# Optimization experiments

Measured on AMD Instinct MI355X. Metric: run time of the kernel, lower is better.

Reference implementation:

```python
import jax, jax.numpy as jnp
import numpy as np

NUM_SEGMENTS = 8192  # number of graphs/segments (B); batch ids are in [0, B)
N = 8388608          # total nodes


def setup_inputs() -> dict:
    key = jax.random.key(0)
    k1, k2 = jax.random.split(key)
    x = jax.random.normal(k1, (N,), dtype=jnp.float32)
    batch = jnp.sort(jax.random.randint(k2, (N,), 0, NUM_SEGMENTS))
    return {"x": x, "batch": batch}


def _sparsemax(x, batch):
    n = x.shape[0]
    # per-segment max subtraction (shift invariance / numerical stability)
    seg_max = jax.ops.segment_max(x, batch, num_segments=NUM_SEGMENTS)
    xs = x - seg_max[batch]

    # segmented descending sort: primary key = batch, secondary = -x
    order = jnp.lexsort((-xs, batch))
    sx = xs[order]          # sorted values, segment-contiguous, descending within segment
    sb = batch[order]       # == sorted batch ids

    # segment sizes and start offsets
    num_nodes = jax.ops.segment_sum(jnp.ones_like(batch), batch, num_segments=NUM_SEGMENTS)
    cum = jnp.concatenate([jnp.zeros((1,), num_nodes.dtype), jnp.cumsum(num_nodes)[:-1]])

    # within-segment 1-based rank (rhos) and within-segment cumsum
    start = cum[sb]
    rhos = (jnp.arange(n) - start + 1).astype(x.dtype)
    c = jnp.cumsum(sx)
    base = jnp.where(start > 0, c[jnp.maximum(start - 1, 0)], jnp.zeros((), x.dtype))
    seg_cumsum = c - base

    # sparsemax support: rho * z_sorted > cumsum - 1
    support = rhos * sx > seg_cumsum - 1.0
    supp_size = jax.ops.segment_sum(support.astype(num_nodes.dtype), sb, num_segments=NUM_SEGMENTS)

    # threshold tau per segment: (cumsum at support boundary - 1) / support_size
    idx = jnp.clip(cum + supp_size - 1, 0, n - 1)
    tau = (seg_cumsum[idx] - 1.0) / jnp.maximum(supp_size, 1).astype(x.dtype)

    return jnp.maximum(xs - tau[batch], 0.0)


def reference(x, batch):
    return _sparsemax(x, batch)
```

## Files before the change

kernel.cpp:

```cpp
#include <hip/hip_runtime.h>


#define NSEG   8192
#define NTOT   8388608
#define L1N    524288
#define L2N    32768
#define L3N    2048
#define PADV   (-3.0e38f)
#define WREG   1216
#define FBB    256

__device__ __forceinline__ int esw(const int e) {
    return (e & ~15) | ((e + (e >> 4)) & 15);
}

__device__ __forceinline__ float sxor(const float v, const int tm) {
    if (tm == 1)
        return __int_as_float(__builtin_amdgcn_mov_dpp(__float_as_int(v), 0xB1, 0xF, 0xF, true));
    if (tm == 2)
        return __int_as_float(__builtin_amdgcn_mov_dpp(__float_as_int(v), 0x4E, 0xF, 0xF, true));
    if (tm == 8)
        return __int_as_float(__builtin_amdgcn_mov_dpp(__float_as_int(v), 0x128, 0xF, 0xF, true));
    return __shfl_xor(v, tm, 64);
}

__device__ __forceinline__ void cs(float& a, float& b, const bool up) {
    const float lo = fminf(a, b), hi = fmaxf(a, b);
    a = up ? hi : lo;
    b = up ? lo : hi;
}
__device__ __forceinline__ void csr(float& a, float& b, const bool up) {
    const bool sw = ((a > b) != up);
    const float t = a;
    a = sw ? b : a;
    b = sw ? t : b;
}

__device__ __forceinline__ void sort4(float r[4], const int gib) {
    cs(r[0], r[1], true);  cs(r[2], r[3], false);
    const bool u4 = ((gib & 4) == 0);
    cs(r[0], r[2], u4); cs(r[1], r[3], u4);
    cs(r[0], r[1], u4); cs(r[2], r[3], u4);
}

template<int K>
__device__ __forceinline__ void bmerge4(float r[4], const int gib) {
    const bool up = ((gib & K) == 0);
    #pragma unroll
    for (int j = K >> 1; j >= 4; j >>= 1) {
        const bool tkm = (up == ((gib & j) == 0));
        const int tm = j >> 2;
        #pragma unroll
        for (int m = 0; m < 4; ++m) {
            const float p = sxor(r[m], tm);
            r[m] = ((r[m] > p) == tkm) ? r[m] : p;
        }
    }
    #pragma unroll
    for (int j = 2; j >= 1; j >>= 1)
        #pragma unroll
        for (int m = 0; m < 4; ++m)
            if ((m & j) == 0) csr(r[m], r[m | j], up);
}

template<int K, int J>
__device__ __forceinline__ void cepm(float r[16]) {
    #pragma unroll
    for (int m = 0; m < 16; ++m)
        if ((m & J) == 0) { const bool up = ((m & K) == 0); cs(r[m], r[m | J], up); }
}
template<int J>
__device__ __forceinline__ void cep(float r[16], const bool up) {
    #pragma unroll
    for (int m = 0; m < 16; ++m)
        if ((m & J) == 0) cs(r[m], r[m | J], up);
}
template<int KD>
__device__ __forceinline__ void kphase16(float r[16], const int l) {
    const bool up = ((l & (KD >> 4)) == 0);
    #pragma unroll
    for (int tm = KD >> 5; tm >= 1; tm >>= 1) {
        const bool tkm = (up == ((l & tm) == 0));
        #pragma unroll
        for (int m = 0; m < 16; ++m) {
            const float p = sxor(r[m], tm);
            r[m] = ((r[m] > p) == tkm) ? r[m] : p;
        }
    }
    if (KD >= 1024) {
        cep<8>(r, up); cep<4>(r, up); cep<2>(r, up); cep<1>(r, up);
    } else {
        #pragma unroll
        for (int j = 8; j >= 1; j >>= 1)
            #pragma unroll
            for (int m = 0; m < 16; ++m)
                if ((m & j) == 0) csr(r[m], r[m | j], up);
    }
}
__device__ __forceinline__ void wsort1024(float r[16], const int l) {
    cepm<2, 1>(r);
    cepm<4, 2>(r); cepm<4, 1>(r);
    cepm<8, 4>(r); cepm<8, 2>(r); cepm<8, 1>(r);
    kphase16<16>(r, l);  kphase16<32>(r, l);  kphase16<64>(r, l);
    kphase16<128>(r, l); kphase16<256>(r, l); kphase16<512>(r, l);
    kphase16<1024>(r, l);
}

__global__ __launch_bounds__(256) void k1_bounds(
    const int* __restrict__ batch, int* __restrict__ starts, const int n)
{
    const int t = blockIdx.x * blockDim.x + threadIdx.x;
    const int i0 = t << 2;
    if (i0 >= n) return;
    const int4 b4 = ((const int4*)batch)[t];
    int bp = __shfl_up(b4.w, 1, 64);
    if (((threadIdx.x & 63) == 0) && i0 > 0) bp = batch[i0 - 1];
    if (i0 == 0) { for (int b = 0; b <= b4.x; ++b) starts[b] = 0; }
    else { for (int b = bp + 1; b <= b4.x; ++b) starts[b] = i0; }
    for (int b = b4.x + 1; b <= b4.y; ++b) starts[b] = i0 + 1;
    for (int b = b4.y + 1; b <= b4.z; ++b) starts[b] = i0 + 2;
    for (int b = b4.z + 1; b <= b4.w; ++b) starts[b] = i0 + 3;
    if (i0 + 4 == n) { for (int b = b4.w + 1; b <= NSEG; ++b) starts[b] = n; }
}

__global__ __launch_bounds__(256) void k2w(
    const float* __restrict__ x, const int* __restrict__ starts,
    float* __restrict__ mx_out, float* __restrict__ S, float* __restrict__ L1)
{
    __shared__ __align__(16) float Wall[4 * WREG];
    const int tid  = threadIdx.x;
    const int lane = tid & 63;
    const int wid  = tid >> 6;
    float* W = Wall + wid * WREG;

    const int b = blockIdx.x * 4 + wid;
    const int s = starts[b], e = starts[b + 1];
    const int n = e - s;
    if (n <= 0) { if (lane == 0) mx_out[b] = 0.0f; return; }

    const bool med = (n > 1024);
    const int  nb  = n - 1024;

    float r[16], rb[4];
    #pragma unroll
    for (int m = 0; m < 16; ++m) { const int i = (m << 6) + lane; r[m] = (i < n) ? x[s + i] : PADV; }
    if (med) {
        #pragma unroll
        for (int m = 0; m < 4; ++m) { const int i = 1024 + (m << 6) + lane; rb[m] = (i < n) ? x[s + i] : PADV; }
    }

    float mx = r[0];
    #pragma unroll
    for (int m = 1; m < 16; ++m) mx = fmaxf(mx, r[m]);
    if (med) {
        #pragma unroll
        for (int m = 0; m < 4; ++m) mx = fmaxf(mx, rb[m]);
    }
    #pragma unroll
    for (int o = 32; o; o >>= 1) mx = fmaxf(mx, sxor(mx, o));
    if (lane == 0) mx_out[b] = mx;

    #pragma unroll
    for (int m = 0; m < 16; ++m) r[m] = r[m] - mx;
    if (med) {
        #pragma unroll
        for (int m = 0; m < 4; ++m) rb[m] = rb[m] - mx;
    }

    wsort1024(r, lane);

    if (med) {
        const int gib = 4 * lane;
        sort4(rb, gib);
        bmerge4<8>(rb, gib);   bmerge4<16>(rb, gib);  bmerge4<32>(rb, gib);
        bmerge4<64>(rb, gib);  bmerge4<128>(rb, gib); bmerge4<256>(rb, gib);

        float tu[16];
        #pragma unroll
        for (int m = 0; m < 16; ++m) {
            const int k  = ((63 - lane) << 4) + (15 - m);
            const int sk = (k >> 2) & 63;
            const float pv = __shfl(rb[(15 - m) & 3], sk, 64);
            const float hi = fmaxf(r[m], pv);
            const float lo = fminf(r[m], pv);
            const bool act = (lane >= 48);
            tu[m] = act ? lo : PADV;
            r[m]  = act ? hi : r[m];
        }
        kphase16<1024>(r, lane);
        #pragma unroll
        for (int tm = 8; tm >= 1; tm >>= 1) {
            const bool tkm = ((lane & tm) == 0);
            #pragma unroll
            for (int m = 0; m < 16; ++m) {
                const float p = sxor(tu[m], tm);
                tu[m] = ((tu[m] > p) == tkm) ? tu[m] : p;
            }
        }
        cep<8>(tu, true); cep<4>(tu, true); cep<2>(tu, true); cep<1>(tu, true);

        #pragma unroll
        for (int m = 0; m < 16; ++m) W[esw(16 * lane + m)] = r[m];
        if (lane >= 48) {
            const int t0 = (lane - 48) << 4;
            #pragma unroll
            for (int m = 0; m < 16; ++m) {
                const int t = t0 + m;
                if (t < nb && t < 192) W[esw(1024 + t)] = tu[m];
            }
        }
    } else {
        #pragma unroll
        for (int m = 0; m < 16; ++m) W[esw(16 * lane + m)] = r[m];
    }

    {
        const int sA = (s + 3) & ~3;
        const int eA = e & ~3;
        if (sA >= eA) {
            for (int i = lane; i < n; i += 64) S[s + i] = W[esw(i)];
        } else {
            if (lane < sA - s) S[s + lane] = W[esw(lane)];
            for (int c = sA + (lane << 2); c < eA; c += 256) {
                const int i = c - s;
                float4 f;
                f.x = W[esw(i)]; f.y = W[esw(i + 1)];
                f.z = W[esw(i + 2)]; f.w = W[esw(i + 3)];
                *(float4*)(S + c) = f;
            }
            if (lane < e - eA) S[eA + lane] = W[esw(eA + lane - s)];
        }
    }

    const int q0 = (s + 15) >> 4, q1 = e >> 4;
    for (int rr = lane; rr < q1 - q0; rr += 64) {
        const int lb = ((q0 + rr) << 4) - s;
        float v[16];
        #pragma unroll
        for (int ii = 0; ii < 16; ++ii) v[ii] = W[esw(lb + ii)];
        float a = 0.0f;
        #pragma unroll
        for (int ii = 0; ii < 16; ++ii) a = a + v[ii];
        L1[q0 + rr] = a;
    }
}

__global__ __launch_bounds__(256) void kM1(
    const float* __restrict__ S, const int* __restrict__ starts,
    float* __restrict__ L1, float* __restrict__ L2, float* __restrict__ L3)
{
    __shared__ float l2s[256];
    __shared__ int sbr[2];
    const int k = blockIdx.x, tid = threadIdx.x;

    if (tid < 2) {
        const int target = 65536 * (k + tid);
        int lo = 0, hi = NSEG;
        while (lo < hi) { const int mid = (lo + hi) >> 1; if (starts[mid] < target) lo = mid + 1; else hi = mid; }
        sbr[tid] = lo;
    }
    __syncthreads();
    for (int b = sbr[0] + tid; b < sbr[1]; b += 256) {
        const int s = starts[b];
        if (s & 15) {
            const int q = s >> 4;
            const float* p = S + ((size_t)q << 4);
            float a = 0.0f;
            #pragma unroll
            for (int i = 0; i < 16; ++i) a = a + p[i];
            L1[q] = a;
        }
    }
    __syncthreads();

    const int q2 = (k << 8) + tid;
    {
        const float* p = L1 + ((size_t)q2 << 4);
        float a = 0.0f;
        #pragma unroll
        for (int i = 0; i < 16; ++i) a = a + p[i];
        L2[q2] = a;
        l2s[tid] = a;
    }
    __syncthreads();
    if (tid < 16) {
        float a = 0.0f;
        #pragma unroll
        for (int i = 0; i < 16; ++i) a = a + l2s[(tid << 4) + i];
        L3[(k << 4) + tid] = a;
    }
}

__global__ __launch_bounds__(256) void kB(const float* __restrict__ L1,
                                          const float* __restrict__ L2,
                                          const float* __restrict__ L3g,
                                          float* __restrict__ C1)
{
    __shared__ float l3[L3N], c3[L3N], l4[128], c4[128], l5[8], c5[8], c2s[256];
    const int k = blockIdx.x, tid = threadIdx.x;

    for (int q = tid; q < L3N; q += 256) l3[q] = L3g[q];
    __syncthreads();
    if (tid < 128) {
        float a = 0.0f;
        for (int i = 0; i < 16; ++i) a = a + l3[tid * 16 + i];
        l4[tid] = a;
    }
    __syncthreads();
    if (tid < 8) {
        float a = 0.0f;
        for (int i = 0; i < 16; ++i) a = a + l4[tid * 16 + i];
        l5[tid] = a;
    }
    __syncthreads();
    if (tid == 0) {
        float a = 0.0f;
        for (int i = 0; i < 8; ++i) { a = a + l5[i]; c5[i] = a; }
    }
    __syncthreads();
    if (tid < 8) {
        const float pre = tid ? c5[tid - 1] : 0.0f;
        float a = 0.0f;
        for (int i = 0; i < 16; ++i) { a = a + l4[tid * 16 + i]; c4[tid * 16 + i] = tid ? (a + pre) : a; }
    }
    __syncthreads();
    if (tid < 128) {
        const float pre = tid ? c4[tid - 1] : 0.0f;
        float a = 0.0f;
        for (int i = 0; i < 16; ++i) { a = a + l3[tid * 16 + i]; c3[tid * 16 + i] = tid ? (a + pre) : a; }
    }
    __syncthreads();
    if (tid < 16) {
        const int q2r = (k << 4) + tid;
        const float pre = q2r ? c3[q2r - 1] : 0.0f;
        const float* p = L2 + ((size_t)q2r << 4);
        float a = 0.0f;
        #pragma unroll
        for (int i = 0; i < 16; ++i) { a = a + p[i]; c2s[(tid << 4) + i] = q2r ? (a + pre) : a; }
    }
    __syncthreads();
    {
        const int p1 = (k << 8) + 1 + tid;
        if (p1 < L2N) {
            const float pre = c2s[tid];
            const float4* pL4 = (const float4*)(L1 + ((size_t)p1 << 4));
            float o[16];
            float a = 0.0f;
            #pragma unroll
            for (int v = 0; v < 4; ++v) {
                const float4 f = pL4[v];
                a = a + f.x; o[4 * v + 0] = a + pre;
                a = a + f.y; o[4 * v + 1] = a + pre;
                a = a + f.z; o[4 * v + 2] = a + pre;
                a = a + f.w; o[4 * v + 3] = a + pre;
            }
            float4* c4p = (float4*)(C1 + ((size_t)p1 << 4));
            #pragma unroll
            for (int v = 0; v < 4; ++v) {
                float4 f;
                f.x = o[4 * v + 0]; f.y = o[4 * v + 1];
                f.z = o[4 * v + 2]; f.w = o[4 * v + 3];
                c4p[v] = f;
            }
        }
        if (k == 0 && tid == 0) {
            float a = 0.0f;
            #pragma unroll
            for (int i = 0; i < 16; ++i) { a = a + L1[i]; C1[i] = a; }
        }
    }
}

__device__ __forceinline__ float c_row(const int j, const float* __restrict__ S,
                                       const float* __restrict__ C1)
{
    const int q = j >> 4;
    const float* p = S + ((size_t)q << 4);
    float a = 0.0f;
    for (int i = 0; i <= (j & 15); ++i) a = a + p[i];
    return q ? (a + C1[q - 1]) : a;
}

__global__ __launch_bounds__(256) void kCF(
    const float* __restrict__ x, const float* __restrict__ S, const float* __restrict__ C1,
    const int* __restrict__ starts, const int* __restrict__ batch,
    const float* __restrict__ mx, float* __restrict__ out)
{
    const int lane = threadIdx.x & 63;
    const int b = blockIdx.x * 4 + (threadIdx.x >> 6);
    const int s = starts[b], e = starts[b + 1];
    const int n = e - s;
    if (n <= 0) return;

    float base = 0.0f;
    if (lane == 0 && s > 0) base = c_row(s - 1, S, C1);
    base = __shfl(base, 0, 64);

    const int q0 = s >> 4;
    const int nrows = ((e - 1) >> 4) - q0 + 1;
    const int R = (nrows < 32) ? nrows : 32;

    int cnt = 0;
    for (int rr = lane; rr < R; rr += 64) {
        const int q = q0 + rr;
        const float pre = q ? C1[q - 1] : 0.0f;
        float vals[16];
        const float4* p4 = (const float4*)(S + ((size_t)q << 4));
        #pragma unroll
        for (int v = 0; v < 4; ++v) {
            const float4 f = p4[v];
            vals[4 * v + 0] = f.x; vals[4 * v + 1] = f.y;
            vals[4 * v + 2] = f.z; vals[4 * v + 3] = f.w;
        }
        float a = 0.0f;
        #pragma unroll
        for (int i = 0; i < 16; ++i) {
            a = a + vals[i];
            const int j = (q << 4) + i;
            if (j >= s && j < e) {
                const float cj  = q ? (a + pre) : a;
                const float seg = (cj - base) - 1.0f;
                const float lhs = (float)(j - s + 1) * vals[i];
                if (lhs > seg) cnt++;
            }
        }
    }
    #pragma unroll
    for (int o = 32; o; o >>= 1) cnt += __shfl_xor(cnt, o, 64);
    const int supp = cnt;

    float t = 0.0f;
    if (lane == 0) {
        if (supp > 0) {
            const int idx = s + supp - 1;
            const float ci = c_row(idx, S, C1);
            t = ((ci - base) - 1.0f) / (float)supp;
        } else {
            const int g  = batch[s - 1];
            const int sg = starts[g];
            const float bg = (sg > 0) ? c_row(sg - 1, S, C1) : 0.0f;
            t = (base - bg) - 1.0f;
        }
    }
    t = __shfl(t, 0, 64);
    const float tb = t;
    const float mxb = mx[b];

    const int sA = (s + 3) & ~3;
    const int eA = e & ~3;
    if (sA >= eA) {
        for (int i = s + lane; i < e; i += 64) {
            float v = x[i] - mxb;
            v = v - tb;
            out[i] = v > 0.0f ? v : 0.0f;
        }
    } else {
        if (lane < sA - s) {
            const int i = s + lane;
            float v = x[i] - mxb;
            v = v - tb;
            out[i] = v > 0.0f ? v : 0.0f;
        }
        for (int c = sA + (lane << 2); c < eA; c += 256) {
            float4 f = *(const float4*)(x + c);
            f.x = f.x - mxb; f.x = f.x - tb; f.x = f.x > 0.0f ? f.x : 0.0f;
            f.y = f.y - mxb; f.y = f.y - tb; f.y = f.y > 0.0f ? f.y : 0.0f;
            f.z = f.z - mxb; f.z = f.z - tb; f.z = f.z > 0.0f ? f.z : 0.0f;
            f.w = f.w - mxb; f.w = f.w - tb; f.w = f.w > 0.0f ? f.w : 0.0f;
            *(float4*)(out + c) = f;
        }
        if (lane < e - eA) {
            const int i = eA + lane;
            float v = x[i] - mxb;
            v = v - tb;
            out[i] = v > 0.0f ? v : 0.0f;
        }
    }
}

__global__ void k_base(const float* __restrict__ S, const float* __restrict__ C1,
                       const int* __restrict__ starts,
                       float* __restrict__ baseA, float* __restrict__ rowP)
{
    const int b = blockIdx.x * blockDim.x + threadIdx.x;
    if (b >= NSEG) return;
    const int s = starts[b];
    float P = 0.0f, base = 0.0f;
    if (s > 0) {
        const int j = s - 1;
        const int q = j >> 4;
        const float* p = S + ((size_t)q << 4);
        float a = 0.0f;
        for (int i = 0; i <= (j & 15); ++i) a = a + p[i];
        if (s & 15) P = a;
        base = q ? (a + C1[q - 1]) : a;
    }
    baseA[b] = base;
    rowP[b] = P;
}

__global__ __launch_bounds__(128) void kC(
    const float* __restrict__ x, const float* __restrict__ S, const float* __restrict__ C1,
    const int* __restrict__ starts, const int* __restrict__ batch,
    const float* __restrict__ mx, const float* __restrict__ baseA,
    const float* __restrict__ rowP, float* __restrict__ out)
{
    __shared__ float stau[1];
    __shared__ int   scnt[2];

    const int b = blockIdx.x, tid = threadIdx.x;
    const int s = starts[b], e = starts[b + 1];
    const int n = e - s;
    if (n <= 0) return;

    const float base = baseA[b];
    const int q0 = s >> 4;
    const int nrows = ((e - 1) >> 4) - q0 + 1;
    const int R = (nrows < 32) ? nrows : 32;

    int cnt = 0;
    for (int rr = tid; rr < R; rr += 128) {
        const int q = q0 + rr;
        const float pre = q ? C1[q - 1] : 0.0f;
        float vals[16];
        const float4* p4 = (const float4*)(S + ((size_t)q << 4));
        #pragma unroll
        for (int v = 0; v < 4; ++v) {
            const float4 f = p4[v];
            vals[4 * v + 0] = f.x; vals[4 * v + 1] = f.y;
            vals[4 * v + 2] = f.z; vals[4 * v + 3] = f.w;
        }
        float a = (rr == 0) ? rowP[b] : 0.0f;
        const int i0 = (rr == 0) ? (s & 15) : 0;
        #pragma unroll
        for (int i = 0; i < 16; ++i) {
            if (i >= i0) {
                a = a + vals[i];
                const int j = (q << 4) + i;
                if (j < e) {
                    const float cj  = q ? (a + pre) : a;
                    const float seg = (cj - base) - 1.0f;
                    const float lhs = (float)(j - s + 1) * vals[i];
                    if (lhs > seg) cnt++;
                }
            }
        }
    }
    #pragma unroll
    for (int o = 32; o; o >>= 1) cnt += __shfl_xor(cnt, o, 64);
    if ((tid & 63) == 0) scnt[tid >> 6] = cnt;
    __syncthreads();
    const int supp = scnt[0] + scnt[1];

    if (tid == 0) {
        float t;
        if (supp > 0) {
            const int idx = s + supp - 1;
            const int qi = idx >> 4;
            const float* p = S + ((size_t)qi << 4);
            float a = (qi == q0) ? rowP[b] : 0.0f;
            const int i0 = (qi == q0) ? (s & 15) : 0;
            for (int i = i0; i <= (idx & 15); ++i) a = a + p[i];
            const float ci = qi ? (a + C1[qi - 1]) : a;
            t = ((ci - base) - 1.0f) / (float)supp;
        } else {
            int idx = s - 1; if (idx < 0) idx = 0;
            const int g = batch[idx];
            t = (base - baseA[g]) - 1.0f;
        }
        stau[0] = t;
    }
    __syncthreads();
    const float tb = stau[0];
    const float mxb = mx[b];
    for (int i = s + tid; i < e; i += 128) {
        float v = x[i] - mxb;
        v = v - tb;
        out[i] = v > 0.0f ? v : 0.0f;
    }
}

__global__ void fb_sparsemax(const float* x, const int* batch, float* out, int n_total)
{
    __shared__ float sred[FBB];
    __shared__ int   sredi[FBB];
    __shared__ int   sb2[2];
    const int tid = threadIdx.x;
    const int b = blockIdx.x;
    if (tid == 0) {
        int lo = 0, hi = n_total;
        while (lo < hi) { int mid = (lo + hi) >> 1; if (batch[mid] < b) lo = mid + 1; else hi = mid; }
        sb2[0] = lo; hi = n_total;
        while (lo < hi) { int mid = (lo + hi) >> 1; if (batch[mid] < b + 1) lo = mid + 1; else hi = mid; }
        sb2[1] = lo;
    }
    __syncthreads();
    const int s = sb2[0], e = sb2[1], n = e - s;
    if (n <= 0) return;
    float mx = -3.0e38f;
    for (int i = s + tid; i < e; i += FBB) { float v = x[i]; if (v > mx) mx = v; }
    sred[tid] = mx; __syncthreads();
    for (int o = FBB / 2; o > 0; o >>= 1) { if (tid < o && sred[tid + o] > sred[tid]) sred[tid] = sred[tid + o]; __syncthreads(); }
    mx = sred[0]; __syncthreads();
    float tau = -1.0f; int prev = -1;
    for (int it = 0; it < 64; ++it) {
        float sum = 0.0f; int cnt = 0;
        for (int i = s + tid; i < e; i += FBB) { float v = x[i] - mx; if (v > tau) { sum += v; cnt++; } }
        sred[tid] = sum; sredi[tid] = cnt; __syncthreads();
        for (int o = FBB / 2; o > 0; o >>= 1) { if (tid < o) { sred[tid] += sred[tid + o]; sredi[tid] += sredi[tid + o]; } __syncthreads(); }
        sum = sred[0]; cnt = sredi[0]; __syncthreads();
        if (cnt == prev || cnt == 0) break;
        tau = (sum - 1.0f) / (float)cnt; prev = cnt; __syncthreads();
    }
    for (int i = s + tid; i < e; i += FBB) { float v = x[i] - mx - tau; out[i] = v > 0.0f ? v : 0.0f; }
}
__global__ void fb_sentinel(float* out) { if (threadIdx.x == 0 && blockIdx.x == 0) out[0] = 20000.0f; }

extern "C" void kernel_launch(void* const* d_in, const int* in_sizes, int n_in,
                              void* d_out, int out_size, void* d_ws, size_t ws_size,
                              hipStream_t stream) {
    const float* x     = (const float*)d_in[0];
    const int*   batch = (const int*)d_in[1];
    float*       out   = (float*)d_out;
    float*       wsf   = (float*)d_ws;
    const int n = in_sizes[0];

    const size_t base_f  = (size_t)8448 + 8192 + L1N + L2N + L3N + L1N;
    const size_t small_f = base_f + 8192 + 8192;
    const size_t big_f   = small_f + (size_t)NTOT;
    if (n != NTOT || ws_size < small_f * sizeof(float)) {
        fb_sparsemax<<<NSEG, FBB, 0, stream>>>(x, batch, out, n);
        fb_sentinel<<<1, 64, 0, stream>>>(out);
        return;
    }
    int*   starts = (int*)wsf;
    float* mx     = wsf + 8448;
    float* L1 = mx + 8192;
    float* L2 = L1 + L1N;
    float* L3 = L2 + L2N;
    float* C1 = L3 + L3N;
    float* baseA = C1 + L1N;
    float* rowP  = baseA + 8192;

    const bool big = (ws_size >= big_f * sizeof(float));
    float* S = big ? (rowP + 8192) : out;

    k1_bounds<<<(n / 4 + 255) / 256, 256, 0, stream>>>(batch, starts, n);
    k2w<<<NSEG / 4, 256, 0, stream>>>(x, starts, mx, S, L1);
    kM1<<<128, 256, 0, stream>>>(S, starts, L1, L2, L3);
    kB<<<128, 256, 0, stream>>>(L1, L2, L3, C1);
    if (big) {
        kCF<<<NSEG / 4, 256, 0, stream>>>(x, S, C1, starts, batch, mx, out);
    } else {
        k_base<<<NSEG / 256, 256, 0, stream>>>(S, C1, starts, baseA, rowP);
        kC<<<NSEG, 128, 0, stream>>>(x, S, C1, starts, batch, mx, baseA, rowP, out);
    }
}
```

Before: 179.9 us.

## Fold segment-bounds kernel into k2w via per-wave binary search on batch

Removes the separate k1_bounds launch, which read the whole batch array to scatter segment start offsets. Each wave of k2w now binary-searches the sorted batch array for its own segment's start and end and writes starts[b] for later kernels. The vectorized float4 store of sorted values to S is also replaced by a plain scalar strided loop. The trade is one less launch and full batch pass against 23 dependent serialized global loads per wave and less efficient stores.

```diff
diff --git a/kernel.cpp b/kernel.cpp
--- a/kernel.cpp
+++ b/kernel.cpp
@@ -106,26 +106,10 @@
     kphase16<1024>(r, l);
 }
 
-__global__ __launch_bounds__(256) void k1_bounds(
-    const int* __restrict__ batch, int* __restrict__ starts, const int n)
-{
-    const int t = blockIdx.x * blockDim.x + threadIdx.x;
-    const int i0 = t << 2;
-    if (i0 >= n) return;
-    const int4 b4 = ((const int4*)batch)[t];
-    int bp = __shfl_up(b4.w, 1, 64);
-    if (((threadIdx.x & 63) == 0) && i0 > 0) bp = batch[i0 - 1];
-    if (i0 == 0) { for (int b = 0; b <= b4.x; ++b) starts[b] = 0; }
-    else { for (int b = bp + 1; b <= b4.x; ++b) starts[b] = i0; }
-    for (int b = b4.x + 1; b <= b4.y; ++b) starts[b] = i0 + 1;
-    for (int b = b4.y + 1; b <= b4.z; ++b) starts[b] = i0 + 2;
-    for (int b = b4.z + 1; b <= b4.w; ++b) starts[b] = i0 + 3;
-    if (i0 + 4 == n) { for (int b = b4.w + 1; b <= NSEG; ++b) starts[b] = n; }
-}
-
 __global__ __launch_bounds__(256) void k2w(
-    const float* __restrict__ x, const int* __restrict__ starts,
-    float* __restrict__ mx_out, float* __restrict__ S, float* __restrict__ L1)
+    const float* __restrict__ x, const int* __restrict__ batch,
+    int* __restrict__ starts, float* __restrict__ mx_out,
+    float* __restrict__ S, float* __restrict__ L1)
 {
     __shared__ __align__(16) float Wall[4 * WREG];
     const int tid  = threadIdx.x;
@@ -134,7 +118,18 @@
     float* W = Wall + wid * WREG;
 
     const int b = blockIdx.x * 4 + wid;
-    const int s = starts[b], e = starts[b + 1];
+
+    int lo0 = 0, hi0 = NTOT, lo1 = 0, hi1 = NTOT;
+    #pragma unroll 1
+    for (int it = 0; it < 23; ++it) {
+        if (lo0 < hi0) { const int m = (lo0 + hi0) >> 1; if (batch[m] < b) lo0 = m + 1; else hi0 = m; }
+        if (lo1 < hi1) { const int m = (lo1 + hi1) >> 1; if (batch[m] < b + 1) lo1 = m + 1; else hi1 = m; }
+    }
+    const int s = lo0, e = lo1;
+    if (lane == 0) {
+        starts[b] = s;
+        if (b == NSEG - 1) starts[NSEG] = NTOT;
+    }
     const int n = e - s;
     if (n <= 0) { if (lane == 0) mx_out[b] = 0.0f; return; }
 
@@ -214,23 +209,7 @@
         for (int m = 0; m < 16; ++m) W[esw(16 * lane + m)] = r[m];
     }
 
-    {
-        const int sA = (s + 3) & ~3;
-        const int eA = e & ~3;
-        if (sA >= eA) {
-            for (int i = lane; i < n; i += 64) S[s + i] = W[esw(i)];
-        } else {
-            if (lane < sA - s) S[s + lane] = W[esw(lane)];
-            for (int c = sA + (lane << 2); c < eA; c += 256) {
-                const int i = c - s;
-                float4 f;
-                f.x = W[esw(i)]; f.y = W[esw(i + 1)];
-                f.z = W[esw(i + 2)]; f.w = W[esw(i + 3)];
-                *(float4*)(S + c) = f;
-            }
-            if (lane < e - eA) S[eA + lane] = W[esw(eA + lane - s)];
-        }
-    }
+    for (int i = lane; i < n; i += 64) S[s + i] = W[esw(i)];
 
     const int q0 = (s + 15) >> 4, q1 = e >> 4;
     for (int rr = lane; rr < q1 - q0; rr += 64) {
@@ -645,8 +624,7 @@
     const bool big = (ws_size >= big_f * sizeof(float));
     float* S = big ? (rowP + 8192) : out;
 
-    k1_bounds<<<(n / 4 + 255) / 256, 256, 0, stream>>>(batch, starts, n);
-    k2w<<<NSEG / 4, 256, 0, stream>>>(x, starts, mx, S, L1);
+    k2w<<<NSEG / 4, 256, 0, stream>>>(x, batch, starts, mx, S, L1);
     kM1<<<128, 256, 0, stream>>>(S, starts, L1, L2, L3);
     kB<<<128, 256, 0, stream>>>(L1, L2, L3, C1);
     if (big) {
```

Result: slower. 188.6 us (+4.8%).
